# Kernel tuning notes

Hardware: AMD Instinct MI355X
Metric: run time of the kernel (lower is better)

Reference implementation:

```python
import jax, jax.numpy as jnp
import numpy as np
from jax.scipy.special import gammaln

B, L, D, H = 4, 2048, 512, 8
HD = D // H
SCALE = HD ** -0.5
TEMP = 1.0
PRIOR = 0.2
THRESH = 0.5
EPS = 1e-6


def setup_inputs() -> dict:
    key = jax.random.key(0)
    ks = jax.random.split(key, 6)
    xav = (6.0 / (D + D)) ** 0.5  # xavier_uniform bound for square Linear
    xav_o = (6.0 / (1 + D)) ** 0.5
    hidden = jax.random.normal(ks[0], (B, L, D), jnp.float32)
    Wq = jax.random.uniform(ks[1], (D, D), jnp.float32, -xav, xav)
    Wk = jax.random.uniform(ks[2], (D, D), jnp.float32, -xav, xav)
    Wv = jax.random.uniform(ks[3], (D, D), jnp.float32, -xav, xav)
    Wo = jax.random.uniform(ks[4], (1, D), jnp.float32, -xav_o, xav_o)
    u = jax.random.uniform(ks[5], (B, L), jnp.float32, EPS, 1.0 - EPS)
    return {"hidden": hidden, "Wq": Wq, "Wk": Wk, "Wv": Wv, "Wo": Wo, "u": u}


def _pool_one(bounds, hid):
    # bounds: [L] float (hard boundaries), hid: [L, D]
    # segment id: token belongs to the group ending at the next boundary
    ids = (jnp.cumsum(bounds) - bounds).astype(jnp.int32)  # [L]
    s = jax.ops.segment_sum(hid, ids, num_segments=L)       # [L, D]
    c = jax.ops.segment_sum(jnp.ones((L,), hid.dtype), ids, num_segments=L)
    return s / jnp.maximum(c, 1.0)[:, None]


def reference(hidden, Wq, Wk, Wv, Wo, u):
    # projections (torch Linear: y = x @ W^T)
    Q = (hidden @ Wq.T).reshape(B, L, H, HD).transpose(0, 2, 1, 3)  # [B,H,L,HD]
    K = (hidden @ Wk.T).reshape(B, L, H, HD).transpose(0, 2, 1, 3)
    V = (hidden @ Wv.T).reshape(B, L, H, HD).transpose(0, 2, 1, 3)

    scores = jnp.einsum('bhqd,bhkd->bhqk', Q, K) * SCALE            # [B,H,L,L]
    attw = jax.nn.softmax(scores, axis=-1)
    att = jnp.einsum('bhqk,bhkd->bhqd', attw, V)                    # [B,H,L,HD]
    att = att.transpose(0, 2, 1, 3).reshape(B, L, D)

    boundary_scores = attw.sum(axis=-1).mean(axis=1)                # [B,L]
    boundary_logits = (att @ Wo.T)[..., 0]                          # [B,L]

    probs = jnp.clip(jax.nn.sigmoid(boundary_logits + boundary_scores), 0.0, 1.0)
    p_logits = jnp.log(probs) - jnp.log1p(-probs)
    noise = jnp.log(u) - jnp.log1p(-u)  # logistic noise (RelaxedBernoulli rsample)
    soft = jax.nn.sigmoid((p_logits + noise) / TEMP)
    hard = (soft > THRESH).astype(soft.dtype)
    hard = hard - jax.lax.stop_gradient(soft) + soft  # straight-through

    pooled = jax.vmap(_pool_one)(hard, hidden)                      # [B,L,D]

    # Binomial(L, prior) log-prob of number of boundaries
    k = hard.sum(axis=-1)
    n = jnp.float32(L)
    logprob = (gammaln(n + 1.0) - gammaln(k + 1.0) - gammaln(n - k + 1.0)
               + k * jnp.log(jnp.float32(PRIOR)) + (n - k) * jnp.log1p(-jnp.float32(PRIOR)))
    loss = -logprob.mean() / n
    return pooled, loss
```

## Files before the change

kernel.cpp:

```cpp
#include <hip/hip_runtime.h>
#include <hip/hip_bf16.h>

#define Bsz 4
#define Lseq 2048
#define Dm 512
#define Hh 8
#define HD 64
#define QBLK 128
#define KT 64
#define NT (Lseq / KT)
#define PNT (Dm / 32)

typedef __attribute__((ext_vector_type(8))) _Float16 f16x8;
typedef __attribute__((ext_vector_type(4))) float f32x4;

__global__ void wvo_kernel(const float* __restrict__ Wv, const float* __restrict__ Wo,
                           float* __restrict__ Wvo) {
    int h = blockIdx.x >> 1;
    int c = (blockIdx.x & 1) * 256 + threadIdx.x;
    float acc = 0.f;
    #pragma unroll 8
    for (int d = 0; d < HD; ++d)
        acc += Wv[(size_t)(h * HD + d) * Dm + c] * Wo[h * HD + d];
    Wvo[h * Dm + c] = acc;
}

__device__ __forceinline__ void split8f(float4 x, float4 y, f16x8& h, f16x8& l) {
    float v[8] = {x.x, x.y, x.z, x.w, y.x, y.y, y.z, y.w};
    #pragma unroll
    for (int j = 0; j < 8; ++j) {
        _Float16 hh = (_Float16)v[j];
        h[j] = hh;
        l[j] = (_Float16)((v[j] - (float)hh) * 2048.0f);
    }
}

__global__ void __launch_bounds__(256, 2) proj_mfma_kernel(
    const float* __restrict__ A,
    const float* __restrict__ Wq, const float* __restrict__ Wk,
    _Float16* __restrict__ Qhp, _Float16* __restrict__ Qlp,
    _Float16* __restrict__ Khp, _Float16* __restrict__ Klp) {
    __shared__ _Float16 AhS[2][128][32];
    __shared__ _Float16 AlS[2][128][32];
    __shared__ _Float16 BhS[2][128][32];
    __shared__ _Float16 BlS[2][128][32];

    int tid = threadIdx.x;
    int lane = tid & 63, wid = tid >> 6;
    int wm = wid >> 1, wn = wid & 1;
    int r = lane & 15, g = lane >> 4;
    int m0 = blockIdx.x * 128;
    int nblk = blockIdx.y;
    bool isQ = nblk < 4;
    const float* Wsrc = isQ ? (Wq + (size_t)nblk * 128 * Dm)
                            : (Wk + (size_t)(nblk - 4) * 128 * Dm);
    _Float16* Hout = isQ ? Qhp : Khp;
    _Float16* Lout = isQ ? Qlp : Klp;
    int ncol0 = (nblk & 3) * 128;

    int c0 = tid * 2, c1 = tid * 2 + 1;
    int ar0 = c0 >> 2, akc0 = c0 & 3;
    int ar1 = c1 >> 2, akc1 = c1 & 3;
    int asw0 = (akc0 ^ ((ar0 >> 1) & 3)) * 8;
    int asw1 = (akc1 ^ ((ar1 >> 1) & 3)) * 8;

    const float* Abase = A + (size_t)m0 * Dm;

    float4 La0, La1, La2, La3, Lb0, Lb1, Lb2, Lb3;

#define PLOAD(T) do { \
    const float* ap0 = Abase + (size_t)ar0 * Dm + (T) * 32 + akc0 * 8; \
    const float* ap1 = Abase + (size_t)ar1 * Dm + (T) * 32 + akc1 * 8; \
    const float* bp0 = Wsrc + (size_t)ar0 * Dm + (T) * 32 + akc0 * 8; \
    const float* bp1 = Wsrc + (size_t)ar1 * Dm + (T) * 32 + akc1 * 8; \
    La0 = *(const float4*)ap0; La1 = *(const float4*)(ap0 + 4); \
    La2 = *(const float4*)ap1; La3 = *(const float4*)(ap1 + 4); \
    Lb0 = *(const float4*)bp0; Lb1 = *(const float4*)(bp0 + 4); \
    Lb2 = *(const float4*)bp1; Lb3 = *(const float4*)(bp1 + 4); \
} while (0)

#define PWRITE(BUF) do { \
    f16x8 hv, lv; \
    split8f(La0, La1, hv, lv); \
    *(f16x8*)&AhS[BUF][ar0][asw0] = hv; *(f16x8*)&AlS[BUF][ar0][asw0] = lv; \
    split8f(La2, La3, hv, lv); \
    *(f16x8*)&AhS[BUF][ar1][asw1] = hv; *(f16x8*)&AlS[BUF][ar1][asw1] = lv; \
    split8f(Lb0, Lb1, hv, lv); \
    *(f16x8*)&BhS[BUF][ar0][asw0] = hv; *(f16x8*)&BlS[BUF][ar0][asw0] = lv; \
    split8f(Lb2, Lb3, hv, lv); \
    *(f16x8*)&BhS[BUF][ar1][asw1] = hv; *(f16x8*)&BlS[BUF][ar1][asw1] = lv; \
} while (0)

    f32x4 acc1[4][4], acc2[4][4];
    #pragma unroll
    for (int mr = 0; mr < 4; ++mr)
        #pragma unroll
        for (int nr = 0; nr < 4; ++nr) {
            acc1[mr][nr] = (f32x4){0.f, 0.f, 0.f, 0.f};
            acc2[mr][nr] = (f32x4){0.f, 0.f, 0.f, 0.f};
        }

    PLOAD(0);
    PWRITE(0);
    __syncthreads();

    int sw8 = (g ^ ((r >> 1) & 3)) * 8;
    for (int t = 0; t < PNT; ++t) {
        int cur = t & 1;
        if (t + 1 < PNT) PLOAD(t + 1);
        f16x8 bhf[4], blf[4];
        #pragma unroll
        for (int nr = 0; nr < 4; ++nr) {
            int row = wn * 64 + nr * 16 + r;
            bhf[nr] = *(const f16x8*)&BhS[cur][row][sw8];
            blf[nr] = *(const f16x8*)&BlS[cur][row][sw8];
        }
        #pragma unroll
        for (int mr = 0; mr < 4; ++mr) {
            int row = wm * 64 + mr * 16 + r;
            f16x8 ah = *(const f16x8*)&AhS[cur][row][sw8];
            f16x8 al = *(const f16x8*)&AlS[cur][row][sw8];
            #pragma unroll
            for (int nr = 0; nr < 4; ++nr) {
                acc1[mr][nr] = __builtin_amdgcn_mfma_f32_16x16x32_f16(ah, bhf[nr], acc1[mr][nr], 0, 0, 0);
                acc2[mr][nr] = __builtin_amdgcn_mfma_f32_16x16x32_f16(ah, blf[nr], acc2[mr][nr], 0, 0, 0);
                acc2[mr][nr] = __builtin_amdgcn_mfma_f32_16x16x32_f16(al, bhf[nr], acc2[mr][nr], 0, 0, 0);
            }
        }
        if (t + 1 < PNT) PWRITE(cur ^ 1);
        __syncthreads();
    }

    #pragma unroll
    for (int mr = 0; mr < 4; ++mr)
        #pragma unroll
        for (int nr = 0; nr < 4; ++nr)
            #pragma unroll
            for (int j = 0; j < 4; ++j) {
                float C = acc1[mr][nr][j] + acc2[mr][nr][j] * (1.0f / 2048.0f);
                size_t m = (size_t)(m0 + wm * 64 + mr * 16 + g * 4 + j);
                size_t n = (size_t)(ncol0 + wn * 64 + nr * 16 + r);
                _Float16 hh = (_Float16)C;
                Hout[m * Dm + n] = hh;
                Lout[m * Dm + n] = (_Float16)((C - (float)hh) * 2048.0f);
            }
#undef PLOAD
#undef PWRITE
}

__global__ void vo_kernel(const float* __restrict__ hidden, const float* __restrict__ Wvo,
                          float* __restrict__ vo) {
    int bh = blockIdx.x;
    int b = bh >> 3, h = bh & 7;
    int l = blockIdx.y * 256 + threadIdx.x;
    __shared__ float w[Dm];
    for (int i = threadIdx.x; i < Dm; i += 256) w[i] = Wvo[h * Dm + i];
    __syncthreads();
    const float* hr = hidden + ((size_t)b * Lseq + l) * Dm;
    float a0 = 0.f, a1 = 0.f, a2 = 0.f, a3 = 0.f;
    #pragma unroll 8
    for (int c = 0; c < Dm; c += 4) {
        float4 v = *(const float4*)(hr + c);
        a0 += v.x * w[c]; a1 += v.y * w[c + 1]; a2 += v.z * w[c + 2]; a3 += v.w * w[c + 3];
    }
    vo[(size_t)bh * Lseq + l] = (a0 + a1) + (a2 + a3);
}

__global__ void __launch_bounds__(256, 2) attn_mfma_kernel(
    const _Float16* __restrict__ Qhp, const _Float16* __restrict__ Qlp,
    const _Float16* __restrict__ Khp, const _Float16* __restrict__ Klp,
    const float* __restrict__ vo, float* __restrict__ blpart) {
    int tid = threadIdx.x;
    int wid = tid >> 6, lane = tid & 63;
    int blk = blockIdx.x;
    int bh = blk & 31;
    int qblk = blk >> 5;
    int b = bh >> 3, h = bh & 7;
    int q0 = qblk * QBLK + wid * 32;
    int r = lane & 15, g = lane >> 4;

    __shared__ _Float16 KhS[2][KT][64];
    __shared__ _Float16 KlS[2][KT][64];
    __shared__ float vos[Lseq];

    const _Float16* Kh_g = Khp + ((size_t)b * Lseq) * Dm + h * HD;
    const _Float16* Kl_g = Klp + ((size_t)b * Lseq) * Dm + h * HD;

    int c0 = tid * 2, c1 = tid * 2 + 1;
    int sr0 = c0 >> 3, so0 = (c0 & 7) * 8;
    int sr1 = c1 >> 3, so1 = (c1 & 7) * 8;
    int dw0 = (so0 ^ ((sr0 & 7) << 3));
    int dw1 = (so1 ^ ((sr1 & 7) << 3));

    f16x8 nh0 = *(const f16x8*)(Kh_g + (size_t)sr0 * Dm + so0);
    f16x8 nh1 = *(const f16x8*)(Kh_g + (size_t)sr1 * Dm + so1);
    f16x8 nl0 = *(const f16x8*)(Kl_g + (size_t)sr0 * Dm + so0);
    f16x8 nl1 = *(const f16x8*)(Kl_g + (size_t)sr1 * Dm + so1);

    f16x8 Qh[2][2], Ql[2][2];
    #pragma unroll
    for (int f = 0; f < 2; ++f) {
        size_t qbase = ((size_t)(b * Lseq + q0 + f * 16 + r)) * Dm + h * HD + g * 8;
        Qh[f][0] = *(const f16x8*)(Qhp + qbase);
        Qh[f][1] = *(const f16x8*)(Qhp + qbase + 32);
        Ql[f][0] = *(const f16x8*)(Qlp + qbase);
        Ql[f][1] = *(const f16x8*)(Qlp + qbase + 32);
    }

    for (int i = tid; i < Lseq; i += 256) vos[i] = vo[(size_t)bh * Lseq + i];

    *(f16x8*)&KhS[0][sr0][dw0] = nh0;
    *(f16x8*)&KhS[0][sr1][dw1] = nh1;
    *(f16x8*)&KlS[0][sr0][dw0] = nl0;
    *(f16x8*)&KlS[0][sr1][dw1] = nl1;
    __syncthreads();

    double Yd[2] = {0.0, 0.0}, Zd[2] = {0.0, 0.0};
    int i0 = (g * 8) ^ ((r & 7) << 3);

    for (int t = 0; t < NT; ++t) {
        int cur = t & 1;
        if (t + 1 < NT) {
            size_t kn = (size_t)(t + 1) * KT;
            nh0 = *(const f16x8*)(Kh_g + (kn + sr0) * Dm + so0);
            nh1 = *(const f16x8*)(Kh_g + (kn + sr1) * Dm + so1);
            nl0 = *(const f16x8*)(Kl_g + (kn + sr0) * Dm + so0);
            nl1 = *(const f16x8*)(Kl_g + (kn + sr1) * Dm + so1);
        }
        #pragma unroll
        for (int s = 0; s < 4; ++s) {
            int row = s * 16 + r;
            f16x8 ah0 = *(const f16x8*)&KhS[cur][row][i0];
            f16x8 ah1 = *(const f16x8*)&KhS[cur][row][i0 ^ 32];
            f16x8 al0 = *(const f16x8*)&KlS[cur][row][i0];
            f16x8 al1 = *(const f16x8*)&KlS[cur][row][i0 ^ 32];
            float4 vkv = *(const float4*)&vos[t * KT + s * 16 + g * 4];
            float vk[4] = {vkv.x, vkv.y, vkv.z, vkv.w};
            #pragma unroll
            for (int f = 0; f < 2; ++f) {
                f32x4 acc1 = {0.f, 0.f, 0.f, 0.f};
                f32x4 acc2 = {0.f, 0.f, 0.f, 0.f};
                acc1 = __builtin_amdgcn_mfma_f32_16x16x32_f16(ah0, Qh[f][0], acc1, 0, 0, 0);
                acc1 = __builtin_amdgcn_mfma_f32_16x16x32_f16(ah1, Qh[f][1], acc1, 0, 0, 0);
                acc2 = __builtin_amdgcn_mfma_f32_16x16x32_f16(ah0, Ql[f][0], acc2, 0, 0, 0);
                acc2 = __builtin_amdgcn_mfma_f32_16x16x32_f16(ah1, Ql[f][1], acc2, 0, 0, 0);
                acc2 = __builtin_amdgcn_mfma_f32_16x16x32_f16(al0, Qh[f][0], acc2, 0, 0, 0);
                acc2 = __builtin_amdgcn_mfma_f32_16x16x32_f16(al1, Qh[f][1], acc2, 0, 0, 0);
                float Ych = 0.f, Zch = 0.f;
                #pragma unroll
                for (int j = 0; j < 4; ++j) {
                    float sv = (acc1[j] + acc2[j] * (1.0f / 2048.0f)) * 0.125f;
                    float e = __expf(sv);
                    Ych += e * vk[j];
                    Zch += e;
                }
                Yd[f] += (double)Ych;
                Zd[f] += (double)Zch;
            }
        }
        if (t + 1 < NT) {
            int nxt = cur ^ 1;
            *(f16x8*)&KhS[nxt][sr0][dw0] = nh0;
            *(f16x8*)&KhS[nxt][sr1][dw1] = nh1;
            *(f16x8*)&KlS[nxt][sr0][dw0] = nl0;
            *(f16x8*)&KlS[nxt][sr1][dw1] = nl1;
        }
        __syncthreads();
    }

    #pragma unroll
    for (int f = 0; f < 2; ++f) {
        double Y = Yd[f], Z = Zd[f];
        Y += __shfl_xor(Y, 16, 64);
        Y += __shfl_xor(Y, 32, 64);
        Z += __shfl_xor(Z, 16, 64);
        Z += __shfl_xor(Z, 32, 64);
        if (lane < 16)
            blpart[(size_t)bh * Lseq + q0 + f * 16 + lane] = (float)(Y / Z);
    }
}

__global__ void blhard_kernel(const float* __restrict__ blpart, const float* __restrict__ u,
                              int* __restrict__ hard) {
    int i = blockIdx.x * 256 + threadIdx.x;
    int b = i >> 11, l = i & (Lseq - 1);
    float bl = 0.f;
    #pragma unroll
    for (int h = 0; h < Hh; ++h)
        bl += blpart[((size_t)(b * Hh + h)) * Lseq + l];
    float x = bl + 1.0f;
    float probs = 1.0f / (1.0f + expf(-x));
    probs = fminf(fmaxf(probs, 0.0f), 1.0f);
    float pl = logf(probs) - log1pf(-probs);
    float un = u[i];
    float noise = logf(un) - log1pf(-un);
    float t = pl + noise;
    float soft = 1.0f / (1.0f + expf(-t));
    hard[i] = (soft > 0.5f) ? 1 : 0;
}

__global__ void scan_kernel(const int* __restrict__ hard, int* __restrict__ segstart,
                            int* __restrict__ segend, int* __restrict__ kcount) {
    int b = blockIdx.x;
    int tid = threadIdx.x;
    __shared__ int hs[Lseq];
    __shared__ int chunk[256];
    for (int i = tid; i < Lseq; i += 256) {
        segstart[b * Lseq + i] = 0;
        segend[b * Lseq + i] = 0;
    }
    int base = b * Lseq;
    int sum = 0;
    int loc[8];
    #pragma unroll
    for (int j = 0; j < 8; ++j) {
        int v = hard[base + tid * 8 + j];
        hs[tid * 8 + j] = v;
        loc[j] = sum;
        sum += v;
    }
    chunk[tid] = sum;
    __syncthreads();
    for (int off = 1; off < 256; off <<= 1) {
        int v = (tid >= off) ? chunk[tid - off] : 0;
        __syncthreads();
        chunk[tid] += v;
        __syncthreads();
    }
    int ebase = chunk[tid] - sum;
    #pragma unroll
    for (int j = 0; j < 8; ++j) {
        int ll = tid * 8 + j;
        int id = ebase + loc[j];
        if (ll == 0 || hs[ll - 1] == 1) segstart[b * Lseq + id] = ll;
        if (ll == Lseq - 1 || hs[ll] == 1) segend[b * Lseq + id] = ll + 1;
    }
    if (tid == 255) kcount[b] = chunk[255];
}

__global__ void pool_kernel(const float* __restrict__ hidden, const int* __restrict__ segstart,
                            const int* __restrict__ segend, float* __restrict__ out) {
    int i = blockIdx.x * 256 + threadIdx.x;
    int d = i & (Dm - 1);
    int s = (i >> 9) & (Lseq - 1);
    int b = i >> 20;
    int st = segstart[b * Lseq + s];
    int en = segend[b * Lseq + s];
    int n = en - st;
    float acc = 0.f;
    for (int l = st; l < en; ++l)
        acc += hidden[((size_t)b * Lseq + l) * Dm + d];
    out[i] = (n > 0) ? acc / (float)n : 0.0f;
}

__global__ void loss_kernel(const int* __restrict__ kcount, float* __restrict__ out) {
    if (threadIdx.x == 0 && blockIdx.x == 0) {
        float n = (float)Lseq;
        float acc = 0.f;
        for (int b = 0; b < Bsz; ++b) {
            float k = (float)kcount[b];
            float lp = lgammaf(n + 1.0f) - lgammaf(k + 1.0f) - lgammaf(n - k + 1.0f)
                     + k * logf(0.2f) + (n - k) * log1pf(-0.2f);
            acc += lp;
        }
        out[(size_t)Bsz * Lseq * Dm] = -(acc / (float)Bsz) / n;
    }
}

extern "C" void kernel_launch(void* const* d_in, const int* in_sizes, int n_in,
                              void* d_out, int out_size, void* d_ws, size_t ws_size,
                              hipStream_t stream) {
    const float* hidden = (const float*)d_in[0];
    const float* Wq = (const float*)d_in[1];
    const float* Wk = (const float*)d_in[2];
    const float* Wv = (const float*)d_in[3];
    const float* Wo = (const float*)d_in[4];
    const float* u  = (const float*)d_in[5];
    float* out = (float*)d_out;

    char* ws = (char*)d_ws;
    size_t off = 0;
    const size_t plane = (size_t)Bsz * Lseq * Dm * sizeof(_Float16);
    _Float16* Qhp = (_Float16*)(ws + off); off += plane;
    _Float16* Qlp = (_Float16*)(ws + off); off += plane;
    _Float16* Khp = (_Float16*)(ws + off); off += plane;
    _Float16* Klp = (_Float16*)(ws + off); off += plane;
    float* Wvo = (float*)(ws + off); off += (size_t)Hh * Dm * 4;
    float* vo = (float*)(ws + off);  off += (size_t)Bsz * Hh * Lseq * 4;
    float* blpart = (float*)(ws + off); off += (size_t)Bsz * Hh * Lseq * 4;
    int* hard = (int*)(ws + off);    off += (size_t)Bsz * Lseq * 4;
    int* segstart = (int*)(ws + off); off += (size_t)Bsz * Lseq * 4;
    int* segend = (int*)(ws + off);  off += (size_t)Bsz * Lseq * 4;
    int* kcount = (int*)(ws + off);  off += 64;

    wvo_kernel<<<dim3(16), dim3(256), 0, stream>>>(Wv, Wo, Wvo);
    proj_mfma_kernel<<<dim3((Bsz * Lseq) / 128, 8), dim3(256), 0, stream>>>(
        hidden, Wq, Wk, Qhp, Qlp, Khp, Klp);
    vo_kernel<<<dim3(Bsz * Hh, Lseq / 256), dim3(256), 0, stream>>>(hidden, Wvo, vo);
    attn_mfma_kernel<<<dim3(32 * (Lseq / QBLK)), dim3(256), 0, stream>>>(
        Qhp, Qlp, Khp, Klp, vo, blpart);
    blhard_kernel<<<dim3((Bsz * Lseq) / 256), dim3(256), 0, stream>>>(blpart, u, hard);
    scan_kernel<<<dim3(Bsz), dim3(256), 0, stream>>>(hard, segstart, segend, kcount);
    pool_kernel<<<dim3((Bsz * Lseq * Dm) / 256), dim3(256), 0, stream>>>(hidden, segstart, segend, out);
    loss_kernel<<<dim3(1), dim3(64), 0, stream>>>(kcount, out);
}
```

Before: 148.0 us.

## Split attention key range across blocks and merge partial sums in blhard

```diff
diff --git a/kernel.cpp b/kernel.cpp
--- a/kernel.cpp
+++ b/kernel.cpp
@@ -8,7 +8,9 @@
 #define HD 64
 #define QBLK 128
 #define KT 64
-#define NT (Lseq / KT)
+#define KSPLIT 2
+#define KHALF (Lseq / KSPLIT)
+#define NTT (KHALF / KT)
 #define PNT (Dm / 32)
 
 typedef __attribute__((ext_vector_type(8))) _Float16 f16x8;
@@ -166,25 +168,28 @@
     vo[(size_t)bh * Lseq + l] = (a0 + a1) + (a2 + a3);
 }
 
-__global__ void __launch_bounds__(256, 2) attn_mfma_kernel(
+__global__ void __launch_bounds__(256, 4) attn_mfma_kernel(
     const _Float16* __restrict__ Qhp, const _Float16* __restrict__ Qlp,
     const _Float16* __restrict__ Khp, const _Float16* __restrict__ Klp,
-    const float* __restrict__ vo, float* __restrict__ blpart) {
+    const float* __restrict__ vo, double* __restrict__ Yp, double* __restrict__ Zp) {
     int tid = threadIdx.x;
     int wid = tid >> 6, lane = tid & 63;
     int blk = blockIdx.x;
     int bh = blk & 31;
-    int qblk = blk >> 5;
+    int rest = blk >> 5;
+    int qblk = rest & 15;
+    int ks = rest >> 4;
     int b = bh >> 3, h = bh & 7;
     int q0 = qblk * QBLK + wid * 32;
+    int k0 = ks * KHALF;
     int r = lane & 15, g = lane >> 4;
 
     __shared__ _Float16 KhS[2][KT][64];
     __shared__ _Float16 KlS[2][KT][64];
-    __shared__ float vos[Lseq];
-
-    const _Float16* Kh_g = Khp + ((size_t)b * Lseq) * Dm + h * HD;
-    const _Float16* Kl_g = Klp + ((size_t)b * Lseq) * Dm + h * HD;
+    __shared__ float vos[KHALF];
+
+    const _Float16* Kh_g = Khp + ((size_t)(b * Lseq + k0)) * Dm + h * HD;
+    const _Float16* Kl_g = Klp + ((size_t)(b * Lseq + k0)) * Dm + h * HD;
 
     int c0 = tid * 2, c1 = tid * 2 + 1;
     int sr0 = c0 >> 3, so0 = (c0 & 7) * 8;
@@ -207,7 +212,7 @@
         Ql[f][1] = *(const f16x8*)(Qlp + qbase + 32);
     }
 
-    for (int i = tid; i < Lseq; i += 256) vos[i] = vo[(size_t)bh * Lseq + i];
+    for (int i = tid; i < KHALF; i += 256) vos[i] = vo[(size_t)bh * Lseq + k0 + i];
 
     *(f16x8*)&KhS[0][sr0][dw0] = nh0;
     *(f16x8*)&KhS[0][sr1][dw1] = nh1;
@@ -217,16 +222,18 @@
 
     double Yd[2] = {0.0, 0.0}, Zd[2] = {0.0, 0.0};
     int i0 = (g * 8) ^ ((r & 7) << 3);
-
-    for (int t = 0; t < NT; ++t) {
+    const float CEXP = 0.18033688011112042f;
+
+    for (int t = 0; t < NTT; ++t) {
         int cur = t & 1;
-        if (t + 1 < NT) {
+        if (t + 1 < NTT) {
             size_t kn = (size_t)(t + 1) * KT;
             nh0 = *(const f16x8*)(Kh_g + (kn + sr0) * Dm + so0);
             nh1 = *(const f16x8*)(Kh_g + (kn + sr1) * Dm + so1);
             nl0 = *(const f16x8*)(Kl_g + (kn + sr0) * Dm + so0);
             nl1 = *(const f16x8*)(Kl_g + (kn + sr1) * Dm + so1);
         }
+        float Yt[2] = {0.f, 0.f}, Zt[2] = {0.f, 0.f};
         #pragma unroll
         for (int s = 0; s < 4; ++s) {
             int row = s * 16 + r;
@@ -249,16 +256,17 @@
                 float Ych = 0.f, Zch = 0.f;
                 #pragma unroll
                 for (int j = 0; j < 4; ++j) {
-                    float sv = (acc1[j] + acc2[j] * (1.0f / 2048.0f)) * 0.125f;
-                    float e = __expf(sv);
+                    float e = exp2f(fmaf(acc2[j], 1.0f / 2048.0f, acc1[j]) * CEXP);
                     Ych += e * vk[j];
                     Zch += e;
                 }
-                Yd[f] += (double)Ych;
-                Zd[f] += (double)Zch;
+                Yt[f] += Ych;
+                Zt[f] += Zch;
             }
         }
-        if (t + 1 < NT) {
+        Yd[0] += (double)Yt[0]; Zd[0] += (double)Zt[0];
+        Yd[1] += (double)Yt[1]; Zd[1] += (double)Zt[1];
+        if (t + 1 < NTT) {
             int nxt = cur ^ 1;
             *(f16x8*)&KhS[nxt][sr0][dw0] = nh0;
             *(f16x8*)&KhS[nxt][sr1][dw1] = nh1;
@@ -275,19 +283,26 @@
         Y += __shfl_xor(Y, 32, 64);
         Z += __shfl_xor(Z, 16, 64);
         Z += __shfl_xor(Z, 32, 64);
-        if (lane < 16)
-            blpart[(size_t)bh * Lseq + q0 + f * 16 + lane] = (float)(Y / Z);
-    }
-}
-
-__global__ void blhard_kernel(const float* __restrict__ blpart, const float* __restrict__ u,
-                              int* __restrict__ hard) {
+        if (lane < 16) {
+            size_t idx = ((size_t)bh * Lseq + q0 + f * 16 + lane) * KSPLIT + ks;
+            Yp[idx] = Y;
+            Zp[idx] = Z;
+        }
+    }
+}
+
+__global__ void blhard_kernel(const double* __restrict__ Yp, const double* __restrict__ Zp,
+                              const float* __restrict__ u, int* __restrict__ hard) {
     int i = blockIdx.x * 256 + threadIdx.x;
     int b = i >> 11, l = i & (Lseq - 1);
     float bl = 0.f;
     #pragma unroll
-    for (int h = 0; h < Hh; ++h)
-        bl += blpart[((size_t)(b * Hh + h)) * Lseq + l];
+    for (int h = 0; h < Hh; ++h) {
+        size_t base = ((size_t)(b * Hh + h) * Lseq + l) * KSPLIT;
+        double Y = Yp[base] + Yp[base + 1];
+        double Z = Zp[base] + Zp[base + 1];
+        bl += (float)(Y / Z);
+    }
     float x = bl + 1.0f;
     float probs = 1.0f / (1.0f + expf(-x));
     probs = fminf(fmaxf(probs, 0.0f), 1.0f);
@@ -387,7 +402,8 @@
     _Float16* Klp = (_Float16*)(ws + off); off += plane;
     float* Wvo = (float*)(ws + off); off += (size_t)Hh * Dm * 4;
     float* vo = (float*)(ws + off);  off += (size_t)Bsz * Hh * Lseq * 4;
-    float* blpart = (float*)(ws + off); off += (size_t)Bsz * Hh * Lseq * 4;
+    double* Yp = (double*)(ws + off); off += (size_t)Bsz * Hh * Lseq * KSPLIT * 8;
+    double* Zp = (double*)(ws + off); off += (size_t)Bsz * Hh * Lseq * KSPLIT * 8;
     int* hard = (int*)(ws + off);    off += (size_t)Bsz * Lseq * 4;
     int* segstart = (int*)(ws + off); off += (size_t)Bsz * Lseq * 4;
     int* segend = (int*)(ws + off);  off += (size_t)Bsz * Lseq * 4;
@@ -397,9 +413,9 @@
     proj_mfma_kernel<<<dim3((Bsz * Lseq) / 128, 8), dim3(256), 0, stream>>>(
         hidden, Wq, Wk, Qhp, Qlp, Khp, Klp);
     vo_kernel<<<dim3(Bsz * Hh, Lseq / 256), dim3(256), 0, stream>>>(hidden, Wvo, vo);
-    attn_mfma_kernel<<<dim3(32 * (Lseq / QBLK)), dim3(256), 0, stream>>>(
-        Qhp, Qlp, Khp, Klp, vo, blpart);
-    blhard_kernel<<<dim3((Bsz * Lseq) / 256), dim3(256), 0, stream>>>(blpart, u, hard);
+    attn_mfma_kernel<<<dim3(32 * (Lseq / QBLK) * KSPLIT), dim3(256), 0, stream>>>(
+        Qhp, Qlp, Khp, Klp, vo, Yp, Zp);
+    blhard_kernel<<<dim3((Bsz * Lseq) / 256), dim3(256), 0, stream>>>(Yp, Zp, u, hard);
     scan_kernel<<<dim3(Bsz), dim3(256), 0, stream>>>(hard, segstart, segend, kcount);
     pool_kernel<<<dim3((Bsz * Lseq * Dm) / 256), dim3(256), 0, stream>>>(hidden, segstart, segend, out);
     loss_kernel<<<dim3(1), dim3(64), 0, stream>>>(kcount, out);
```

Measured after the change: 151.9 us. 1.03x slower.
